# Performance work log

Hardware: AMD Instinct MI355X
Metric: run time of the kernel (lower is better)

Reference implementation:

```python
import jax, jax.numpy as jnp
import numpy as np

MIN_NORM = 1e-15
BALL_EPS = 4e-3  # torch float32 ball epsilon in KGEmb
E, R, D = 500000, 1000, 256
NQ = 200000
INIT = 1e-3
SCALE = float(1.0 / np.sqrt(D))


def setup_inputs() -> dict:
    key = jax.random.key(0)
    ks = jax.random.split(key, 7)
    heads = jax.random.randint(ks[0], (NQ, 1), 0, E)
    rels = jax.random.randint(ks[1], (NQ, 1), 0, R)
    tails = jax.random.randint(ks[2], (NQ, 1), 0, E)
    queries = jnp.concatenate([heads, rels, tails], axis=1)
    return {
        "queries": queries,
        "entity_emb": INIT * jax.random.normal(ks[3], (E, D), jnp.float32),
        "rel_emb": INIT * jax.random.normal(ks[4], (R, 2 * D), jnp.float32),
        "bias_head": jnp.zeros((E, 1), jnp.float32),
        "bias_tail": jnp.zeros((E, 1), jnp.float32),
        "c": jnp.ones((R, 1), jnp.float32),
        "att_rel_emb": 2.0 * jax.random.uniform(ks[5], (R, 2 * D), jnp.float32) - 1.0,
        "context_emb": INIT * jax.random.normal(ks[6], (R, D), jnp.float32),
    }


def artanh(x):
    x = jnp.clip(x, -1.0 + 1e-5, 1.0 - 1e-5)
    return 0.5 * (jnp.log1p(x) - jnp.log1p(-x))


def givens_rotations(r, x):
    # r, x: [n, d]; operate on d/2 independent 2-vectors
    n, d = x.shape
    g = r.reshape(n, d // 2, 2)
    g = g / jnp.maximum(jnp.linalg.norm(g, axis=-1, keepdims=True), MIN_NORM)
    xr = x.reshape(n, d // 2, 2)
    rot = jnp.stack(
        [g[..., 0] * xr[..., 0] - g[..., 1] * xr[..., 1],
         g[..., 0] * xr[..., 1] + g[..., 1] * xr[..., 0]], axis=-1)
    return rot.reshape(n, d)


def givens_reflection(r, x):
    n, d = x.shape
    g = r.reshape(n, d // 2, 2)
    g = g / jnp.maximum(jnp.linalg.norm(g, axis=-1, keepdims=True), MIN_NORM)
    xr = x.reshape(n, d // 2, 2)
    ref = jnp.stack(
        [g[..., 0] * xr[..., 0] + g[..., 1] * xr[..., 1],
         g[..., 1] * xr[..., 0] - g[..., 0] * xr[..., 1]], axis=-1)
    return ref.reshape(n, d)


def project(x, c):
    norm = jnp.maximum(jnp.linalg.norm(x, axis=-1, keepdims=True), MIN_NORM)
    maxnorm = (1.0 - BALL_EPS) / jnp.sqrt(c)
    return jnp.where(norm > maxnorm, x / norm * maxnorm, x)


def expmap0(u, c):
    sqrt_c = jnp.sqrt(c)
    u_norm = jnp.maximum(jnp.linalg.norm(u, axis=-1, keepdims=True), MIN_NORM)
    gamma_1 = jnp.tanh(sqrt_c * u_norm) * u / (sqrt_c * u_norm)
    return project(gamma_1, c)


def mobius_add(x, y, c):
    x2 = jnp.sum(x * x, axis=-1, keepdims=True)
    y2 = jnp.sum(y * y, axis=-1, keepdims=True)
    xy = jnp.sum(x * y, axis=-1, keepdims=True)
    num = (1.0 + 2.0 * c * xy + c * y2) * x + (1.0 - c * x2) * y
    denom = 1.0 + 2.0 * c * xy + (c ** 2) * x2 * y2
    return num / jnp.maximum(denom, MIN_NORM)


def hyp_distance(x, v, c):
    # x: point on ball, v: Euclidean (tangent) embedding; train mode (paired rows)
    sqrt_c = jnp.sqrt(c)
    vnorm = jnp.maximum(jnp.linalg.norm(v, axis=-1, keepdims=True), MIN_NORM)
    xv = jnp.sum(x * v / vnorm, axis=-1, keepdims=True)
    gamma = jnp.tanh(sqrt_c * vnorm) / vnorm
    x2 = jnp.sum(x * x, axis=-1, keepdims=True)
    c1 = 1.0 - 2.0 * c * gamma * xv + c * gamma ** 2
    c2 = 1.0 - c * x2
    num = jnp.sqrt(jnp.maximum((c1 ** 2) * x2 + (c2 ** 2) * (gamma ** 2)
                               - 2.0 * c1 * c2 * gamma * xv, 0.0))
    denom = jnp.maximum(1.0 - 2.0 * c * gamma * xv + (c ** 2) * (gamma ** 2) * x2, MIN_NORM)
    return 2.0 * artanh(sqrt_c * num / denom) / sqrt_c


def atth_forward(queries, entity_emb, rel_emb, bias_head, bias_tail, c,
                 att_rel_emb, context_emb):
    h, r, t = queries[:, 0], queries[:, 1], queries[:, 2]
    c_q = jax.nn.softplus(c[r])                       # [n, 1]
    head = entity_emb[h]                              # [n, D]
    rot_mat, ref_mat = jnp.split(att_rel_emb[r], 2, axis=1)
    rot_q = givens_rotations(rot_mat, head)           # [n, D]
    ref_q = givens_reflection(ref_mat, head)          # [n, D]
    cands = jnp.stack([ref_q, rot_q], axis=1)         # [n, 2, D]
    ctx = context_emb[r][:, None, :]                  # [n, 1, D]
    att_w = jax.nn.softmax(
        jnp.sum(ctx * cands * SCALE, axis=-1, keepdims=True), axis=1)  # [n, 2, 1]
    att_q = jnp.sum(att_w * cands, axis=1)            # [n, D]
    lhs = expmap0(att_q, c_q)
    rel = jnp.split(rel_emb[r], 2, axis=1)[0]
    rel = expmap0(rel, c_q)
    res = project(mobius_add(lhs, rel, c_q), c_q)
    dist2 = hyp_distance(res, entity_emb[t], c_q) ** 2
    predictions = bias_head[h] + bias_tail[t] + dist2  # [n, 1]
    factors = (head, rel_emb[r], entity_emb[t])
    return (predictions,) + factors


def reference(queries, entity_emb, rel_emb, bias_head, bias_tail, c,
              att_rel_emb, context_emb):
    return atth_forward(queries, entity_emb, rel_emb, bias_head, bias_tail, c,
                        att_rel_emb, context_emb)
```

## Files before the change

kernel.cpp:

```cpp
#include <hip/hip_runtime.h>
#include <math.h>

#define MIN_NORM 1e-15f
#define BALL_EPS 0.004f

constexpr int D  = 256;
constexpr int NQ = 200000;
constexpr float SCALE = 0.0625f;

__device__ __forceinline__ float wave_sum(float v) {
    #pragma unroll
    for (int off = 32; off > 0; off >>= 1) v += __shfl_xor(v, off, 64);
    return v;
}

__device__ __forceinline__ void nt_store4(float* p, float4 v) {
    __builtin_nontemporal_store(v.x, p + 0);
    __builtin_nontemporal_store(v.y, p + 1);
    __builtin_nontemporal_store(v.z, p + 2);
    __builtin_nontemporal_store(v.w, p + 3);
}

__global__ __launch_bounds__(256) void atth_kernel(
    const int*   __restrict__ queries,
    const float* __restrict__ entity_emb,
    const float* __restrict__ rel_emb,
    const float* __restrict__ bias_head,
    const float* __restrict__ bias_tail,
    const float* __restrict__ c_arr,
    const float* __restrict__ att_rel_emb,
    const float* __restrict__ context_emb,
    float*       __restrict__ out)
{
    const int wave = threadIdx.x >> 6;
    const int lane = threadIdx.x & 63;
    const int q = blockIdx.x * 4 + wave;
    if (q >= NQ) return;

    const int h = queries[q * 3 + 0];
    const int r = queries[q * 3 + 1];
    const int t = queries[q * 3 + 2];

    const float craw = c_arr[r];
    const float c = (craw > 20.0f) ? craw : log1pf(expf(craw));
    const float sqrt_c = sqrtf(c);

    const int e4 = lane * 4;

    const float4 head = *(const float4*)(entity_emb  + (size_t)h * D       + e4);
    const float4 tail = *(const float4*)(entity_emb  + (size_t)t * D       + e4);
    const float4 rel0 = *(const float4*)(rel_emb     + (size_t)r * 2 * D       + e4);
    const float4 rel1 = *(const float4*)(rel_emb     + (size_t)r * 2 * D + D   + e4);
    const float4 rotm = *(const float4*)(att_rel_emb + (size_t)r * 2 * D       + e4);
    const float4 refm = *(const float4*)(att_rel_emb + (size_t)r * 2 * D + D   + e4);
    const float4 ctx  = *(const float4*)(context_emb + (size_t)r * D       + e4);

    const float hd[4]  = {head.x, head.y, head.z, head.w};
    const float tl[4]  = {tail.x, tail.y, tail.z, tail.w};
    const float rm[4]  = {rotm.x, rotm.y, rotm.z, rotm.w};
    const float fm[4]  = {refm.x, refm.y, refm.z, refm.w};
    const float cx[4]  = {ctx.x,  ctx.y,  ctx.z,  ctx.w};
    const float rl[4]  = {rel0.x, rel0.y, rel0.z, rel0.w};

    float rq[4], fq[4];
    #pragma unroll
    for (int p = 0; p < 2; ++p) {
        const int i0 = 2 * p, i1 = 2 * p + 1;
        float g0 = rm[i0], g1 = rm[i1];
        float n  = fmaxf(sqrtf(g0 * g0 + g1 * g1), MIN_NORM);
        g0 /= n; g1 /= n;
        rq[i0] = g0 * hd[i0] - g1 * hd[i1];
        rq[i1] = g0 * hd[i1] + g1 * hd[i0];
        float e0 = fm[i0], e1 = fm[i1];
        float m  = fmaxf(sqrtf(e0 * e0 + e1 * e1), MIN_NORM);
        e0 /= m; e1 /= m;
        fq[i0] = e0 * hd[i0] + e1 * hd[i1];
        fq[i1] = e1 * hd[i0] - e0 * hd[i1];
    }

    float sref = 0.0f, srot = 0.0f;
    #pragma unroll
    for (int j = 0; j < 4; ++j) { sref += cx[j] * fq[j]; srot += cx[j] * rq[j]; }
    sref = wave_sum(sref) * SCALE;
    srot = wave_sum(srot) * SCALE;
    const float mx = fmaxf(sref, srot);
    const float eref = expf(sref - mx), erot = expf(srot - mx);
    const float inv_se = 1.0f / (eref + erot);
    const float wref = eref * inv_se, wrot = erot * inv_se;

    float att[4];
    #pragma unroll
    for (int j = 0; j < 4; ++j) att[j] = wref * fq[j] + wrot * rq[j];

    const float maxnorm = (1.0f - BALL_EPS) / sqrt_c;

    float s = 0.0f;
    #pragma unroll
    for (int j = 0; j < 4; ++j) s += att[j] * att[j];
    float un = fmaxf(sqrtf(wave_sum(s)), MIN_NORM);
    float fac = tanhf(sqrt_c * un) / (sqrt_c * un);
    float lhs[4];
    #pragma unroll
    for (int j = 0; j < 4; ++j) lhs[j] = fac * att[j];
    s = 0.0f;
    #pragma unroll
    for (int j = 0; j < 4; ++j) s += lhs[j] * lhs[j];
    float nrm = fmaxf(sqrtf(wave_sum(s)), MIN_NORM);
    if (nrm > maxnorm) {
        const float sc = maxnorm / nrm;
        #pragma unroll
        for (int j = 0; j < 4; ++j) lhs[j] *= sc;
    }

    s = 0.0f;
    #pragma unroll
    for (int j = 0; j < 4; ++j) s += rl[j] * rl[j];
    un = fmaxf(sqrtf(wave_sum(s)), MIN_NORM);
    fac = tanhf(sqrt_c * un) / (sqrt_c * un);
    float rh[4];
    #pragma unroll
    for (int j = 0; j < 4; ++j) rh[j] = fac * rl[j];
    s = 0.0f;
    #pragma unroll
    for (int j = 0; j < 4; ++j) s += rh[j] * rh[j];
    nrm = fmaxf(sqrtf(wave_sum(s)), MIN_NORM);
    if (nrm > maxnorm) {
        const float sc = maxnorm / nrm;
        #pragma unroll
        for (int j = 0; j < 4; ++j) rh[j] *= sc;
    }

    float sx = 0.0f, sy = 0.0f, sxy = 0.0f;
    #pragma unroll
    for (int j = 0; j < 4; ++j) { sx += lhs[j] * lhs[j]; sy += rh[j] * rh[j]; sxy += lhs[j] * rh[j]; }
    const float x2  = wave_sum(sx);
    const float y2  = wave_sum(sy);
    const float xy  = wave_sum(sxy);
    const float ka  = 1.0f + 2.0f * c * xy + c * y2;
    const float kb  = 1.0f - c * x2;
    const float den = fmaxf(1.0f + 2.0f * c * xy + c * c * x2 * y2, MIN_NORM);
    float res[4];
    #pragma unroll
    for (int j = 0; j < 4; ++j) res[j] = (ka * lhs[j] + kb * rh[j]) / den;

    s = 0.0f;
    #pragma unroll
    for (int j = 0; j < 4; ++j) s += res[j] * res[j];
    nrm = fmaxf(sqrtf(wave_sum(s)), MIN_NORM);
    if (nrm > maxnorm) {
        const float sc = maxnorm / nrm;
        #pragma unroll
        for (int j = 0; j < 4; ++j) res[j] *= sc;
    }

    float sv = 0.0f, sxv = 0.0f, sxx = 0.0f;
    #pragma unroll
    for (int j = 0; j < 4; ++j) { sv += tl[j] * tl[j]; sxv += res[j] * tl[j]; sxx += res[j] * res[j]; }
    const float vnorm = fmaxf(sqrtf(wave_sum(sv)), MIN_NORM);
    const float xv    = wave_sum(sxv) / vnorm;
    const float rx2   = wave_sum(sxx);
    const float gamma = tanhf(sqrt_c * vnorm) / vnorm;
    const float c1 = 1.0f - 2.0f * c * gamma * xv + c * gamma * gamma;
    const float c2 = 1.0f - c * rx2;
    const float num = sqrtf(fmaxf(c1 * c1 * rx2 + c2 * c2 * gamma * gamma
                                  - 2.0f * c1 * c2 * gamma * xv, 0.0f));
    const float dden = fmaxf(1.0f - 2.0f * c * gamma * xv
                             + c * c * gamma * gamma * rx2, MIN_NORM);
    float arg = sqrt_c * num / dden;
    arg = fminf(fmaxf(arg, -1.0f + 1e-5f), 1.0f - 1e-5f);
    const float ath  = 0.5f * (log1pf(arg) - log1pf(-arg));
    const float dist = 2.0f * ath / sqrt_c;
    const float dist2 = dist * dist;

    float* out_pred = out;
    float* out_head = out + (size_t)NQ;
    float* out_rel  = out + (size_t)NQ + (size_t)NQ * D;
    float* out_tail = out + (size_t)NQ + (size_t)NQ * D + (size_t)NQ * 2 * D;

    if (lane == 0) {
        __builtin_nontemporal_store(bias_head[h] + bias_tail[t] + dist2, out_pred + q);
    }
    nt_store4(out_head + (size_t)q * D     + e4, head);
    nt_store4(out_rel  + (size_t)q * 2 * D     + e4, rel0);
    nt_store4(out_rel  + (size_t)q * 2 * D + D + e4, rel1);
    nt_store4(out_tail + (size_t)q * D     + e4, tail);
}

extern "C" void kernel_launch(void* const* d_in, const int* in_sizes, int n_in,
                              void* d_out, int out_size, void* d_ws, size_t ws_size,
                              hipStream_t stream) {
    const int*   queries     = (const int*)  d_in[0];
    const float* entity_emb  = (const float*)d_in[1];
    const float* rel_emb     = (const float*)d_in[2];
    const float* bias_head   = (const float*)d_in[3];
    const float* bias_tail   = (const float*)d_in[4];
    const float* c_arr       = (const float*)d_in[5];
    const float* att_rel_emb = (const float*)d_in[6];
    const float* context_emb = (const float*)d_in[7];
    float* out = (float*)d_out;

    const int queries_per_block = 4;
    const int grid = (NQ + queries_per_block - 1) / queries_per_block;
    atth_kernel<<<grid, 256, 0, stream>>>(queries, entity_emb, rel_emb,
                                          bias_head, bias_tail, c_arr,
                                          att_rel_emb, context_emb, out);
}
```

Baseline: 367.0 us.

## Use half-wave per query and reduce norms algebraically to two batched reductions

Each query is now handled by 32 lanes with 8 elements per lane, so a block of 256 threads serves 8 queries instead of 4. The chain of serial wave reductions (expmap, project, mobius add, distance) is replaced by scalar algebra over a few dot products, computed in two batched 5-step shuffle reductions. Output copies are issued before the math, and fast intrinsics (__expf, __logf, rsqrtf, custom tanh) replace the libm calls. The aim is to cut shuffle latency and instruction count in a mostly memory-bound kernel. The cost is more registers per lane and slightly different floating-point rounding.

```diff
diff --git a/kernel.cpp b/kernel.cpp
--- a/kernel.cpp
+++ b/kernel.cpp
@@ -7,18 +7,32 @@
 constexpr int D  = 256;
 constexpr int NQ = 200000;
 constexpr float SCALE = 0.0625f;
-
-__device__ __forceinline__ float wave_sum(float v) {
-    #pragma unroll
-    for (int off = 32; off > 0; off >>= 1) v += __shfl_xor(v, off, 64);
-    return v;
-}
 
 __device__ __forceinline__ void nt_store4(float* p, float4 v) {
     __builtin_nontemporal_store(v.x, p + 0);
     __builtin_nontemporal_store(v.y, p + 1);
     __builtin_nontemporal_store(v.z, p + 2);
     __builtin_nontemporal_store(v.w, p + 3);
+}
+
+__device__ __forceinline__ void half_sum4(float& a, float& b, float& c, float& d) {
+    #pragma unroll
+    for (int off = 16; off > 0; off >>= 1) {
+        a += __shfl_xor(a, off, 64);
+        b += __shfl_xor(b, off, 64);
+        c += __shfl_xor(c, off, 64);
+        d += __shfl_xor(d, off, 64);
+    }
+}
+
+__device__ __forceinline__ void unpack8(float4 a, float4 b, float* d) {
+    d[0] = a.x; d[1] = a.y; d[2] = a.z; d[3] = a.w;
+    d[4] = b.x; d[5] = b.y; d[6] = b.z; d[7] = b.w;
+}
+
+__device__ __forceinline__ float tanh_pos(float x) {
+    const float e = __expf(-2.0f * x);
+    return (1.0f - e) / (1.0f + e);
 }
 
 __global__ __launch_bounds__(256) void atth_kernel(
@@ -32,158 +46,149 @@
     const float* __restrict__ context_emb,
     float*       __restrict__ out)
 {
-    const int wave = threadIdx.x >> 6;
     const int lane = threadIdx.x & 63;
-    const int q = blockIdx.x * 4 + wave;
-    if (q >= NQ) return;
-
-    const int h = queries[q * 3 + 0];
-    const int r = queries[q * 3 + 1];
-    const int t = queries[q * 3 + 2];
-
-    const float craw = c_arr[r];
-    const float c = (craw > 20.0f) ? craw : log1pf(expf(craw));
-    const float sqrt_c = sqrtf(c);
-
-    const int e4 = lane * 4;
-
-    const float4 head = *(const float4*)(entity_emb  + (size_t)h * D       + e4);
-    const float4 tail = *(const float4*)(entity_emb  + (size_t)t * D       + e4);
-    const float4 rel0 = *(const float4*)(rel_emb     + (size_t)r * 2 * D       + e4);
-    const float4 rel1 = *(const float4*)(rel_emb     + (size_t)r * 2 * D + D   + e4);
-    const float4 rotm = *(const float4*)(att_rel_emb + (size_t)r * 2 * D       + e4);
-    const float4 refm = *(const float4*)(att_rel_emb + (size_t)r * 2 * D + D   + e4);
-    const float4 ctx  = *(const float4*)(context_emb + (size_t)r * D       + e4);
-
-    const float hd[4]  = {head.x, head.y, head.z, head.w};
-    const float tl[4]  = {tail.x, tail.y, tail.z, tail.w};
-    const float rm[4]  = {rotm.x, rotm.y, rotm.z, rotm.w};
-    const float fm[4]  = {refm.x, refm.y, refm.z, refm.w};
-    const float cx[4]  = {ctx.x,  ctx.y,  ctx.z,  ctx.w};
-    const float rl[4]  = {rel0.x, rel0.y, rel0.z, rel0.w};
-
-    float rq[4], fq[4];
-    #pragma unroll
-    for (int p = 0; p < 2; ++p) {
-        const int i0 = 2 * p, i1 = 2 * p + 1;
-        float g0 = rm[i0], g1 = rm[i1];
-        float n  = fmaxf(sqrtf(g0 * g0 + g1 * g1), MIN_NORM);
-        g0 /= n; g1 /= n;
-        rq[i0] = g0 * hd[i0] - g1 * hd[i1];
-        rq[i1] = g0 * hd[i1] + g1 * hd[i0];
-        float e0 = fm[i0], e1 = fm[i1];
-        float m  = fmaxf(sqrtf(e0 * e0 + e1 * e1), MIN_NORM);
-        e0 /= m; e1 /= m;
-        fq[i0] = e0 * hd[i0] + e1 * hd[i1];
-        fq[i1] = e1 * hd[i0] - e0 * hd[i1];
-    }
-
-    float sref = 0.0f, srot = 0.0f;
-    #pragma unroll
-    for (int j = 0; j < 4; ++j) { sref += cx[j] * fq[j]; srot += cx[j] * rq[j]; }
-    sref = wave_sum(sref) * SCALE;
-    srot = wave_sum(srot) * SCALE;
-    const float mx = fmaxf(sref, srot);
-    const float eref = expf(sref - mx), erot = expf(srot - mx);
-    const float inv_se = 1.0f / (eref + erot);
-    const float wref = eref * inv_se, wrot = erot * inv_se;
-
-    float att[4];
-    #pragma unroll
-    for (int j = 0; j < 4; ++j) att[j] = wref * fq[j] + wrot * rq[j];
-
-    const float maxnorm = (1.0f - BALL_EPS) / sqrt_c;
-
-    float s = 0.0f;
-    #pragma unroll
-    for (int j = 0; j < 4; ++j) s += att[j] * att[j];
-    float un = fmaxf(sqrtf(wave_sum(s)), MIN_NORM);
-    float fac = tanhf(sqrt_c * un) / (sqrt_c * un);
-    float lhs[4];
-    #pragma unroll
-    for (int j = 0; j < 4; ++j) lhs[j] = fac * att[j];
-    s = 0.0f;
-    #pragma unroll
-    for (int j = 0; j < 4; ++j) s += lhs[j] * lhs[j];
-    float nrm = fmaxf(sqrtf(wave_sum(s)), MIN_NORM);
-    if (nrm > maxnorm) {
-        const float sc = maxnorm / nrm;
-        #pragma unroll
-        for (int j = 0; j < 4; ++j) lhs[j] *= sc;
-    }
-
-    s = 0.0f;
-    #pragma unroll
-    for (int j = 0; j < 4; ++j) s += rl[j] * rl[j];
-    un = fmaxf(sqrtf(wave_sum(s)), MIN_NORM);
-    fac = tanhf(sqrt_c * un) / (sqrt_c * un);
-    float rh[4];
-    #pragma unroll
-    for (int j = 0; j < 4; ++j) rh[j] = fac * rl[j];
-    s = 0.0f;
-    #pragma unroll
-    for (int j = 0; j < 4; ++j) s += rh[j] * rh[j];
-    nrm = fmaxf(sqrtf(wave_sum(s)), MIN_NORM);
-    if (nrm > maxnorm) {
-        const float sc = maxnorm / nrm;
-        #pragma unroll
-        for (int j = 0; j < 4; ++j) rh[j] *= sc;
-    }
-
-    float sx = 0.0f, sy = 0.0f, sxy = 0.0f;
-    #pragma unroll
-    for (int j = 0; j < 4; ++j) { sx += lhs[j] * lhs[j]; sy += rh[j] * rh[j]; sxy += lhs[j] * rh[j]; }
-    const float x2  = wave_sum(sx);
-    const float y2  = wave_sum(sy);
-    const float xy  = wave_sum(sxy);
-    const float ka  = 1.0f + 2.0f * c * xy + c * y2;
-    const float kb  = 1.0f - c * x2;
-    const float den = fmaxf(1.0f + 2.0f * c * xy + c * c * x2 * y2, MIN_NORM);
-    float res[4];
-    #pragma unroll
-    for (int j = 0; j < 4; ++j) res[j] = (ka * lhs[j] + kb * rh[j]) / den;
-
-    s = 0.0f;
-    #pragma unroll
-    for (int j = 0; j < 4; ++j) s += res[j] * res[j];
-    nrm = fmaxf(sqrtf(wave_sum(s)), MIN_NORM);
-    if (nrm > maxnorm) {
-        const float sc = maxnorm / nrm;
-        #pragma unroll
-        for (int j = 0; j < 4; ++j) res[j] *= sc;
-    }
-
-    float sv = 0.0f, sxv = 0.0f, sxx = 0.0f;
-    #pragma unroll
-    for (int j = 0; j < 4; ++j) { sv += tl[j] * tl[j]; sxv += res[j] * tl[j]; sxx += res[j] * res[j]; }
-    const float vnorm = fmaxf(sqrtf(wave_sum(sv)), MIN_NORM);
-    const float xv    = wave_sum(sxv) / vnorm;
-    const float rx2   = wave_sum(sxx);
-    const float gamma = tanhf(sqrt_c * vnorm) / vnorm;
-    const float c1 = 1.0f - 2.0f * c * gamma * xv + c * gamma * gamma;
-    const float c2 = 1.0f - c * rx2;
-    const float num = sqrtf(fmaxf(c1 * c1 * rx2 + c2 * c2 * gamma * gamma
-                                  - 2.0f * c1 * c2 * gamma * xv, 0.0f));
-    const float dden = fmaxf(1.0f - 2.0f * c * gamma * xv
-                             + c * c * gamma * gamma * rx2, MIN_NORM);
-    float arg = sqrt_c * num / dden;
-    arg = fminf(fmaxf(arg, -1.0f + 1e-5f), 1.0f - 1e-5f);
-    const float ath  = 0.5f * (log1pf(arg) - log1pf(-arg));
-    const float dist = 2.0f * ath / sqrt_c;
-    const float dist2 = dist * dist;
+    const int hl   = lane & 31;
+    const int qid  = blockIdx.x * 8 + (threadIdx.x >> 5);
+    if (qid >= NQ) return;
+
+    const int h = queries[qid * 3 + 0];
+    const int r = queries[qid * 3 + 1];
+    const int t = queries[qid * 3 + 2];
+
+    const float craw   = c_arr[r];
+    const float cq     = fmaxf(craw, 0.0f) + log1pf(__expf(-fabsf(craw)));
+    const float sqrt_c = sqrtf(cq);
+
+    const int e8 = hl * 8;
+
+    const float* eh = entity_emb  + (size_t)h * D     + e8;
+    const float* et = entity_emb  + (size_t)t * D     + e8;
+    const float* rr = rel_emb     + (size_t)r * 2 * D + e8;
+    const float* am = att_rel_emb + (size_t)r * 2 * D + e8;
+    const float* cb = context_emb + (size_t)r * D     + e8;
+
+    const float4 h0 = *(const float4*)(eh);     const float4 h1 = *(const float4*)(eh + 4);
+    const float4 t0 = *(const float4*)(et);     const float4 t1 = *(const float4*)(et + 4);
+    const float4 r0 = *(const float4*)(rr);     const float4 r1 = *(const float4*)(rr + 4);
+    const float4 r2 = *(const float4*)(rr + D); const float4 r3 = *(const float4*)(rr + D + 4);
+    const float4 m0 = *(const float4*)(am);     const float4 m1 = *(const float4*)(am + 4);
+    const float4 f0 = *(const float4*)(am + D); const float4 f1 = *(const float4*)(am + D + 4);
+    const float4 ct0 = *(const float4*)(cb);    const float4 ct1 = *(const float4*)(cb + 4);
 
     float* out_pred = out;
     float* out_head = out + (size_t)NQ;
     float* out_rel  = out + (size_t)NQ + (size_t)NQ * D;
     float* out_tail = out + (size_t)NQ + (size_t)NQ * D + (size_t)NQ * 2 * D;
 
-    if (lane == 0) {
-        __builtin_nontemporal_store(bias_head[h] + bias_tail[t] + dist2, out_pred + q);
-    }
-    nt_store4(out_head + (size_t)q * D     + e4, head);
-    nt_store4(out_rel  + (size_t)q * 2 * D     + e4, rel0);
-    nt_store4(out_rel  + (size_t)q * 2 * D + D + e4, rel1);
-    nt_store4(out_tail + (size_t)q * D     + e4, tail);
+    nt_store4(out_head + (size_t)qid * D         + e8,     h0);
+    nt_store4(out_head + (size_t)qid * D         + e8 + 4, h1);
+    nt_store4(out_rel  + (size_t)qid * 2 * D     + e8,     r0);
+    nt_store4(out_rel  + (size_t)qid * 2 * D     + e8 + 4, r1);
+    nt_store4(out_rel  + (size_t)qid * 2 * D + D + e8,     r2);
+    nt_store4(out_rel  + (size_t)qid * 2 * D + D + e8 + 4, r3);
+    nt_store4(out_tail + (size_t)qid * D         + e8,     t0);
+    nt_store4(out_tail + (size_t)qid * D         + e8 + 4, t1);
+
+    float hd[8], tl[8], rl[8], rm[8], fm[8], cx[8];
+    unpack8(h0, h1, hd);
+    unpack8(t0, t1, tl);
+    unpack8(r0, r1, rl);
+    unpack8(m0, m1, rm);
+    unpack8(f0, f1, fm);
+    unpack8(ct0, ct1, cx);
+
+    float rq[8], fq[8];
+    #pragma unroll
+    for (int p = 0; p < 4; ++p) {
+        const int i0 = 2 * p, i1 = 2 * p + 1;
+        float s   = rm[i0] * rm[i0] + rm[i1] * rm[i1];
+        float inv = rsqrtf(fmaxf(s, 1e-30f));
+        const float g0 = rm[i0] * inv, g1 = rm[i1] * inv;
+        rq[i0] = g0 * hd[i0] - g1 * hd[i1];
+        rq[i1] = g0 * hd[i1] + g1 * hd[i0];
+        s   = fm[i0] * fm[i0] + fm[i1] * fm[i1];
+        inv = rsqrtf(fmaxf(s, 1e-30f));
+        const float e0 = fm[i0] * inv, e1 = fm[i1] * inv;
+        fq[i0] = e0 * hd[i0] + e1 * hd[i1];
+        fq[i1] = e1 * hd[i0] - e0 * hd[i1];
+    }
+
+    float sref = 0.0f, srot = 0.0f, url2 = 0.0f, sv = 0.0f;
+    #pragma unroll
+    for (int j = 0; j < 8; ++j) {
+        sref += cx[j] * fq[j];
+        srot += cx[j] * rq[j];
+        url2 += rl[j] * rl[j];
+        sv   += tl[j] * tl[j];
+    }
+    half_sum4(sref, srot, url2, sv);
+    sref *= SCALE; srot *= SCALE;
+
+    const float mx   = fmaxf(sref, srot);
+    const float eref = __expf(sref - mx), erot = __expf(srot - mx);
+    const float inv_se = 1.0f / (eref + erot);
+    const float wref = eref * inv_se, wrot = erot * inv_se;
+
+    float att[8];
+    #pragma unroll
+    for (int j = 0; j < 8; ++j) att[j] = wref * fq[j] + wrot * rq[j];
+
+    float u2 = 0.0f, adr = 0.0f, atl = 0.0f, rtl = 0.0f;
+    #pragma unroll
+    for (int j = 0; j < 8; ++j) {
+        u2  += att[j] * att[j];
+        adr += att[j] * rl[j];
+        atl += att[j] * tl[j];
+        rtl += rl[j]  * tl[j];
+    }
+    half_sum4(u2, adr, atl, rtl);
+
+    const float maxnorm = (1.0f - BALL_EPS) / sqrt_c;
+
+    const float u    = fmaxf(sqrtf(u2), MIN_NORM);
+    const float facA = tanh_pos(sqrt_c * u) / (sqrt_c * u);
+    const float nA   = facA * u;
+    const float sA   = facA * ((nA > maxnorm) ? maxnorm / nA : 1.0f);
+    const float x2   = sA * sA * u2;
+
+    const float url  = fmaxf(sqrtf(url2), MIN_NORM);
+    const float facB = tanh_pos(sqrt_c * url) / (sqrt_c * url);
+    const float nB   = facB * url;
+    const float sB   = facB * ((nB > maxnorm) ? maxnorm / nB : 1.0f);
+    const float y2   = sB * sB * url2;
+
+    const float xy = sA * sB * adr;
+
+    const float ka  = 1.0f + 2.0f * cq * xy + cq * y2;
+    const float kb  = 1.0f - cq * x2;
+    const float den = fmaxf(1.0f + 2.0f * cq * xy + cq * cq * x2 * y2, MIN_NORM);
+    const float pA  = ka * sA / den;
+    const float pB  = kb * sB / den;
+
+    const float rn2 = pA * pA * u2 + 2.0f * pA * pB * adr + pB * pB * url2;
+    const float nrm = fmaxf(sqrtf(rn2), MIN_NORM);
+    const float pr  = (nrm > maxnorm) ? maxnorm / nrm : 1.0f;
+    const float rx2 = rn2 * pr * pr;
+
+    const float vnorm = fmaxf(sqrtf(sv), MIN_NORM);
+    const float sxv   = (pA * atl + pB * rtl) * pr;
+    const float xv    = sxv / vnorm;
+    const float gamma = tanh_pos(sqrt_c * vnorm) / vnorm;
+    const float k1 = 1.0f - 2.0f * cq * gamma * xv + cq * gamma * gamma;
+    const float k2 = 1.0f - cq * rx2;
+    const float num = sqrtf(fmaxf(k1 * k1 * rx2 + k2 * k2 * gamma * gamma
+                                  - 2.0f * k1 * k2 * gamma * xv, 0.0f));
+    const float dden = fmaxf(1.0f - 2.0f * cq * gamma * xv
+                             + cq * cq * gamma * gamma * rx2, MIN_NORM);
+    float arg = sqrt_c * num / dden;
+    arg = fminf(fmaxf(arg, -1.0f + 1e-5f), 1.0f - 1e-5f);
+    const float ath  = 0.5f * __logf((1.0f + arg) / (1.0f - arg));
+    const float dist = 2.0f * ath / sqrt_c;
+    const float dist2 = dist * dist;
+
+    if (hl == 0) {
+        __builtin_nontemporal_store(bias_head[h] + bias_tail[t] + dist2, out_pred + qid);
+    }
 }
 
 extern "C" void kernel_launch(void* const* d_in, const int* in_sizes, int n_in,
@@ -199,7 +204,7 @@
     const float* context_emb = (const float*)d_in[7];
     float* out = (float*)d_out;
 
-    const int queries_per_block = 4;
+    const int queries_per_block = 8;
     const int grid = (NQ + queries_per_block - 1) / queries_per_block;
     atth_kernel<<<grid, 256, 0, stream>>>(queries, entity_emb, rel_emb,
                                           bias_head, bias_tail, c_arr,
```

After: 351.0 us. 1.05x faster.
